# Optimization experiments

Hardware: AMD Instinct MI355X
Metric: run time of the kernel (lower is better)

The kernel has to match this reference:

```python
import jax, jax.numpy as jnp
import numpy as np

D = 512

def _linear(x, W, b):
    # torch Linear: x @ W.T + b, W is [out, in]
    return jnp.einsum('bnd,od->bno', x, W) + b

def _attend(Q, K, V):
    # scores: [B, N, N]
    s = jnp.einsum('bnd,bmd->bnm', Q, K)
    a = jax.nn.softmax(s, axis=-1)
    # F.normalize(p=1, dim=-1): divide by sum of abs (softmax is nonneg, sums to 1,
    # but stay faithful to the original math)
    a = a / jnp.clip(jnp.sum(jnp.abs(a), axis=-1, keepdims=True), 1e-12)
    a = a / jnp.sqrt(jnp.asarray(D, a.dtype))
    return jnp.einsum('bnm,bmd->bnd', a, V)

def setup_inputs() -> dict:
    key = jax.random.key(0)
    ks = jax.random.split(key, 12)
    B, N = 2, 4096
    lim = 1.0 / np.sqrt(D)
    lim2 = 1.0 / np.sqrt(2 * D)
    return {
        'x_f': jax.random.normal(ks[0], (B, N, D), jnp.float32),
        'x_s': jax.random.normal(ks[1], (B, N, D), jnp.float32),
        'Wq': jax.random.uniform(ks[2], (D, D), jnp.float32, -lim, lim),
        'bq': jax.random.uniform(ks[3], (D,), jnp.float32, -lim, lim),
        'Wk': jax.random.uniform(ks[4], (D, D), jnp.float32, -lim, lim),
        'bk': jax.random.uniform(ks[5], (D,), jnp.float32, -lim, lim),
        'Wv': jax.random.uniform(ks[6], (D, D), jnp.float32, -lim, lim),
        'bv': jax.random.uniform(ks[7], (D,), jnp.float32, -lim, lim),
        'Wc': jax.random.uniform(ks[8], (D, 2 * D), jnp.float32, -lim2, lim2),
        'bc': jax.random.uniform(ks[9], (D,), jnp.float32, -lim2, lim2),
    }

def reference(x_f, x_s, Wq, bq, Wk, bk, Wv, bv, Wc, bc):
    # dropout layers are identity in eval mode
    co_occur = jax.nn.relu(_linear(jnp.concatenate([x_f, x_s], axis=-1), Wc, bc))
    # f -> s direction
    out_f = _attend(_linear(x_f, Wq, bq), _linear(x_s, Wk, bk), _linear(x_f, Wv, bv)) + co_occur
    # s -> f direction
    out_s = _attend(_linear(x_s, Wq, bq), _linear(x_f, Wk, bk), _linear(x_s, Wv, bv)) + co_occur
    return (out_f, out_s)
```

## Files before the change

kernel.cpp:

```cpp
#include <hip/hip_runtime.h>
#include <stdint.h>


using bf16x8 = __attribute__((ext_vector_type(8))) short;
using f32x4  = __attribute__((ext_vector_type(4))) float;

typedef __attribute__((address_space(1))) const void as1_void_t;
typedef __attribute__((address_space(3))) void as3_void_t;

__device__ __forceinline__ void gload16(const void* g, void* l) {
  __builtin_amdgcn_global_load_lds((as1_void_t*)g, (as3_void_t*)l, 16, 0, 0);
}

#define BAR_VM0()                                                  \
  do {                                                             \
    asm volatile("s_waitcnt vmcnt(0) lgkmcnt(0)" ::: "memory");    \
    __builtin_amdgcn_s_barrier();                                  \
    __builtin_amdgcn_sched_barrier(0);                             \
  } while (0)

#define BAR_LGKM()                                                 \
  do {                                                             \
    asm volatile("s_waitcnt lgkmcnt(0)" ::: "memory");             \
    __builtin_amdgcn_s_barrier();                                  \
    __builtin_amdgcn_sched_barrier(0);                             \
  } while (0)

__device__ __forceinline__ unsigned f2bf_u(float f) {
  unsigned u = __float_as_uint(f);
  return (u + 0x7fffu + ((u >> 16) & 1u)) >> 16;
}

#define MFMA_BF16(a, b, c) __builtin_amdgcn_mfma_f32_16x16x32_bf16((a), (b), (c), 0, 0, 0)

__global__ void cvt_bf16(const float* __restrict__ src,
                         unsigned short* __restrict__ dst, int n4) {
  int i = blockIdx.x * blockDim.x + threadIdx.x;
  if (i >= n4) return;
  float4 v = ((const float4*)src)[i];
  uint2 o;
  o.x = f2bf_u(v.x) | (f2bf_u(v.y) << 16);
  o.y = f2bf_u(v.z) | (f2bf_u(v.w) << 16);
  ((uint2*)dst)[i] = o;
}

__global__ void split_wc(const float* __restrict__ Wc,
                         unsigned short* __restrict__ Wf,
                         unsigned short* __restrict__ Ws) {
  int t = blockIdx.x * blockDim.x + threadIdx.x;
  int row = t >> 7, col = (t & 127) * 4;
  float4 a = *(const float4*)(Wc + row * 1024 + col);
  float4 b = *(const float4*)(Wc + row * 1024 + 512 + col);
  uint2 oa, ob;
  oa.x = f2bf_u(a.x) | (f2bf_u(a.y) << 16);
  oa.y = f2bf_u(a.z) | (f2bf_u(a.w) << 16);
  ob.x = f2bf_u(b.x) | (f2bf_u(b.y) << 16);
  ob.y = f2bf_u(b.z) | (f2bf_u(b.w) << 16);
  *(uint2*)(Wf + row * 512 + col) = oa;
  *(uint2*)(Ws + row * 512 + col) = ob;
}

template<int EPI>
__global__ void __launch_bounds__(256)
gemm_proj(const unsigned short* __restrict__ A1,
          const unsigned short* __restrict__ A2,
          const unsigned short* __restrict__ W1,
          const unsigned short* __restrict__ W2,
          const float* __restrict__ bias,
          void* __restrict__ Cout, int nk) {
  __shared__ __align__(16) unsigned short As[2][128 * 32];
  __shared__ __align__(16) unsigned short Bs[2][128 * 32];
  const int tid = threadIdx.x;
  const int w = tid >> 6, lane = tid & 63;
  const int m0 = blockIdx.x * 128, n0 = blockIdx.y * 128;
  const int wm = (w >> 1) * 64, wn = (w & 1) * 64;
  f32x4 acc[4][4] = {};

  auto stage = [&](int ks, int bi) {
    const unsigned short* Ab = (EPI == 2 && ks >= 16) ? A2 : A1;
    const unsigned short* Wb = (EPI == 2 && ks >= 16) ? W2 : W1;
    const int k0 = (EPI == 2) ? ((ks & 15) * 32) : (ks * 32);
#pragma unroll
    for (int t = 0; t < 2; ++t) {
      const int o = t * 256 + tid;
      const int row = o >> 2, seg = o & 3;
      gload16(Ab + (size_t)(m0 + row) * 512 + k0 + seg * 8,
              (char*)As[bi] + t * 4096 + w * 1024);
      gload16(Wb + (size_t)(n0 + row) * 512 + k0 + seg * 8,
              (char*)Bs[bi] + t * 4096 + w * 1024);
    }
  };

  stage(0, 0);
  for (int ks = 0; ks < nk; ++ks) {
    const int bi = ks & 1;
    BAR_VM0();
    if (ks + 1 < nk) stage(ks + 1, bi ^ 1);
    bf16x8 a[4], b[4];
#pragma unroll
    for (int i = 0; i < 4; ++i) {
      a[i] = *(const bf16x8*)(As[bi] + (wm + i * 16 + (lane & 15)) * 32 + (lane >> 4) * 8);
      b[i] = *(const bf16x8*)(Bs[bi] + (wn + i * 16 + (lane & 15)) * 32 + (lane >> 4) * 8);
    }
#pragma unroll
    for (int i = 0; i < 4; ++i)
#pragma unroll
      for (int j = 0; j < 4; ++j)
        acc[i][j] = MFMA_BF16(a[i], b[j], acc[i][j]);
  }

  const int lm = lane >> 4, ln = lane & 15;
  if (EPI == 0) {
    unsigned short* Cb = (unsigned short*)Cout;
#pragma unroll
    for (int i = 0; i < 4; ++i)
#pragma unroll
      for (int j = 0; j < 4; ++j) {
        const int col = n0 + wn + j * 16 + ln;
        const float bv = bias[col];
#pragma unroll
        for (int r = 0; r < 4; ++r) {
          const int row = m0 + wm + i * 16 + lm * 4 + r;
          Cb[(size_t)row * 512 + col] = (unsigned short)f2bf_u(acc[i][j][r] + bv);
        }
      }
  } else if (EPI == 1) {
    unsigned short* Cb = (unsigned short*)Cout;
#pragma unroll
    for (int i = 0; i < 4; ++i)
#pragma unroll
      for (int j = 0; j < 4; ++j) {
        const int col = n0 + wn + j * 16 + ln;
        const float bv = bias[col];
#pragma unroll
        for (int r = 0; r < 4; ++r) {
          const int row = m0 + wm + i * 16 + lm * 4 + r;
          const int sb = row >> 12, n = row & 4095;
          Cb[(size_t)(sb * 512 + col) * 4096 + n] = (unsigned short)f2bf_u(acc[i][j][r] + bv);
        }
      }
  } else {
    float* Cb = (float*)Cout;
#pragma unroll
    for (int i = 0; i < 4; ++i)
#pragma unroll
      for (int j = 0; j < 4; ++j) {
        const int col = n0 + wn + j * 16 + ln;
        const float bv = bias[col];
#pragma unroll
        for (int r = 0; r < 4; ++r) {
          const int row = m0 + wm + i * 16 + lm * 4 + r;
          float v = acc[i][j][r] + bv;
          Cb[(size_t)row * 512 + col] = v > 0.f ? v : 0.f;
        }
      }
  }
}

__global__ void __launch_bounds__(512)
flash_attn(const unsigned short* __restrict__ Qb,
           const unsigned short* __restrict__ Kb,
           const unsigned short* __restrict__ Vt,
           const float* __restrict__ CO,
           float* __restrict__ Out) {
  __shared__ __align__(16) unsigned short Ks[2][32 * 512];
  __shared__ __align__(16) unsigned short Vs[2][512 * 32];
  __shared__ __align__(16) float S_lds[64 * 36];
  __shared__ __align__(16) unsigned short P_lds[64 * 48];
  __shared__ __align__(16) float m_run[64];
  __shared__ __align__(16) float l_run[64];
  __shared__ __align__(16) float alpha_l[64];

  const int tid = threadIdx.x;
  const int w = tid >> 6, lane = tid & 63;
  const int q0 = blockIdx.x * 64;
  const int b = blockIdx.y, dir = blockIdx.z;
  const int qw = w >> 1, kw = w & 1;

  const size_t qbase  = (size_t)(dir * 2 + b) * 4096 * 512;
  const size_t kbase  = (size_t)((1 - dir) * 2 + b) * 4096 * 512;
  const size_t vbase  = (size_t)(dir * 2 + b) * 512 * 4096;
  const size_t cobase = (size_t)b * 4096 * 512;
  const size_t obase  = qbase;

  auto stage_tiles = [&](int kt, int bi) {
    const int kv0 = kt * 32;
#pragma unroll
    for (int t = 0; t < 4; ++t) {
      const int krow = t * 8 + w;
      gload16(Kb + kbase + (size_t)(kv0 + krow) * 512 + (lane ^ (krow & 7)) * 8,
              (char*)Ks[bi] + krow * 1024);
      const int dbase = (t * 8 + w) * 16;
      const int d = dbase + (lane >> 2);
      gload16(Vt + vbase + (size_t)d * 4096 + kv0 + (((lane & 3) ^ (d & 3)) * 8),
              (char*)Vs[bi] + dbase * 64);
    }
  };

  if (tid < 64) { m_run[tid] = -1e30f; l_run[tid] = 0.0f; }

  stage_tiles(0, 0);

  bf16x8 qf[16];
  {
    const int qrow = q0 + qw * 16 + (lane & 15);
#pragma unroll
    for (int g = 0; g < 16; ++g)
      qf[g] = *(const bf16x8*)(Qb + qbase + (size_t)qrow * 512 + g * 32 + (lane >> 4) * 8);
  }

  f32x4 o_acc[4][4] = {};

  for (int kt = 0; kt < 128; ++kt) {
    const int bi = kt & 1;
    const unsigned short* Kc = Ks[bi];
    const unsigned short* Vc = Vs[bi];

    BAR_VM0();
    if (kt < 127) stage_tiles(kt + 1, bi ^ 1);

    {
      const int krow = kw * 16 + (lane & 15);
      f32x4 s0 = {}, s1 = {};
#pragma unroll
      for (int g = 0; g < 8; ++g) {
        const int c0 = (g * 4 + (lane >> 4)) ^ (krow & 7);
        const int c1 = ((g + 8) * 4 + (lane >> 4)) ^ (krow & 7);
        bf16x8 k0 = *(const bf16x8*)((const char*)Kc + krow * 1024 + c0 * 16);
        bf16x8 k1 = *(const bf16x8*)((const char*)Kc + krow * 1024 + c1 * 16);
        s0 = MFMA_BF16(qf[g], k0, s0);
        s1 = MFMA_BF16(qf[g + 8], k1, s1);
      }
      const int col = kw * 16 + (lane & 15);
      const int rb = qw * 16 + (lane >> 4) * 4;
#pragma unroll
      for (int r = 0; r < 4; ++r)
        S_lds[(rb + r) * 36 + col] = s0[r] + s1[r];
    }
    BAR_LGKM();

    {
      const int row = w * 8 + (lane >> 3);
      const int j = lane & 7;
      f32x4 sv = *(const f32x4*)&S_lds[row * 36 + j * 4];
      float mx = fmaxf(fmaxf(sv[0], sv[1]), fmaxf(sv[2], sv[3]));
      mx = fmaxf(mx, __shfl_xor(mx, 1));
      mx = fmaxf(mx, __shfl_xor(mx, 2));
      mx = fmaxf(mx, __shfl_xor(mx, 4));
      const float mold = m_run[row];
      const float mnew = fmaxf(mold, mx);
      float p0 = __expf(sv[0] - mnew), p1 = __expf(sv[1] - mnew);
      float p2 = __expf(sv[2] - mnew), p3 = __expf(sv[3] - mnew);
      float ls = p0 + p1 + p2 + p3;
      ls += __shfl_xor(ls, 1);
      ls += __shfl_xor(ls, 2);
      ls += __shfl_xor(ls, 4);
      const float alpha = __expf(mold - mnew);
      if (j == 0) {
        m_run[row] = mnew;
        l_run[row] = l_run[row] * alpha + ls;
        alpha_l[row] = alpha;
      }
      uint2 pw;
      pw.x = f2bf_u(p0) | (f2bf_u(p1) << 16);
      pw.y = f2bf_u(p2) | (f2bf_u(p3) << 16);
      *(uint2*)(P_lds + row * 48 + j * 4) = pw;
    }
    BAR_LGKM();

#pragma unroll
    for (int qi = 0; qi < 4; ++qi) {
      bf16x8 pa = *(const bf16x8*)(P_lds + (qi * 16 + (lane & 15)) * 48 + (lane >> 4) * 8);
      f32x4 al4 = *(const f32x4*)&alpha_l[qi * 16 + (lane >> 4) * 4];
#pragma unroll
      for (int di = 0; di < 4; ++di)
        o_acc[qi][di] *= al4;
#pragma unroll
      for (int di = 0; di < 4; ++di) {
        const int d = w * 64 + di * 16 + (lane & 15);
        const int slot = (lane >> 4) ^ (d & 3);
        bf16x8 vf = *(const bf16x8*)((const char*)Vc + d * 64 + slot * 16);
        o_acc[qi][di] = MFMA_BF16(pa, vf, o_acc[qi][di]);
      }
    }
  }

  BAR_LGKM();

  const float rsd = 0.04419417382415922f;
#pragma unroll
  for (int qi = 0; qi < 4; ++qi) {
#pragma unroll
    for (int r = 0; r < 4; ++r) {
      const int ql = qi * 16 + (lane >> 4) * 4 + r;
      const float inv = rsd / l_run[ql];
      const size_t rowoff = (size_t)(q0 + ql) * 512;
#pragma unroll
      for (int di = 0; di < 4; ++di) {
        const int d = w * 64 + di * 16 + (lane & 15);
        Out[obase + rowoff + d] = o_acc[qi][di][r] * inv + CO[cobase + rowoff + d];
      }
    }
  }
}

extern "C" void kernel_launch(void* const* d_in, const int* in_sizes, int n_in,
                              void* d_out, int out_size, void* d_ws, size_t ws_size,
                              hipStream_t stream) {
  const float* x_f = (const float*)d_in[0];
  const float* x_s = (const float*)d_in[1];
  const float* Wq  = (const float*)d_in[2];
  const float* bq  = (const float*)d_in[3];
  const float* Wk  = (const float*)d_in[4];
  const float* bk  = (const float*)d_in[5];
  const float* Wv  = (const float*)d_in[6];
  const float* bv  = (const float*)d_in[7];
  const float* Wc  = (const float*)d_in[8];
  const float* bc  = (const float*)d_in[9];
  float* out = (float*)d_out;

  unsigned short* Xb  = (unsigned short*)d_ws;
  unsigned short* Qb  = Xb + 8388608;
  unsigned short* Kb  = Qb + 8388608;
  unsigned short* Vt  = Kb + 8388608;
  float*          CO  = (float*)(Vt + 8388608);
  unsigned short* Wqb = (unsigned short*)(CO + 4194304);
  unsigned short* Wkb = Wqb + 262144;
  unsigned short* Wvb = Wkb + 262144;
  unsigned short* Wcf = Wvb + 262144;
  unsigned short* Wcs = Wcf + 262144;

  cvt_bf16<<<4096, 256, 0, stream>>>(x_f, Xb, 1048576);
  cvt_bf16<<<4096, 256, 0, stream>>>(x_s, Xb + 4194304, 1048576);
  cvt_bf16<<<256, 256, 0, stream>>>(Wq, Wqb, 65536);
  cvt_bf16<<<256, 256, 0, stream>>>(Wk, Wkb, 65536);
  cvt_bf16<<<256, 256, 0, stream>>>(Wv, Wvb, 65536);
  split_wc<<<256, 256, 0, stream>>>(Wc, Wcf, Wcs);

  dim3 gQ(128, 4);
  gemm_proj<0><<<gQ, 256, 0, stream>>>(Xb, nullptr, Wqb, nullptr, bq, Qb, 16);
  gemm_proj<0><<<gQ, 256, 0, stream>>>(Xb, nullptr, Wkb, nullptr, bk, Kb, 16);
  gemm_proj<1><<<gQ, 256, 0, stream>>>(Xb, nullptr, Wvb, nullptr, bv, Vt, 16);
  dim3 gC(64, 4);
  gemm_proj<2><<<gC, 256, 0, stream>>>(Xb, Xb + 4194304, Wcf, Wcs, bc, CO, 32);

  dim3 gF(64, 2, 2);
  flash_attn<<<gF, 512, 0, stream>>>(Qb, Kb, Vt, CO, out);
}
```

Measured before the change: 490.2 us.

## Halve flash-attention query tile, split QK over head-dim halves, load V directly

Shrinks the attention block from 64 to 32 query rows, which doubles the grid to 256 blocks and requests 4 blocks per CU via launch bounds. The QK^T product is split across two waves per tile along the head dimension, with partial scores summed in LDS. V fragments are now read straight from global memory into registers instead of being staged in double-buffered LDS, and K is single-buffered. Together these cut LDS and register use to raise occupancy. The cost is that each K/V tile is reread by twice as many blocks, V loads are exposed with no prefetch, and the K prefetch is serialised behind a barrier.

Result: slower. 640.6 us (+30.7%).

```diff
diff --git a/kernel.cpp b/kernel.cpp
--- a/kernel.cpp
+++ b/kernel.cpp
@@ -157,25 +157,24 @@
   }
 }
 
-__global__ void __launch_bounds__(512)
+__global__ void __launch_bounds__(512, 4)
 flash_attn(const unsigned short* __restrict__ Qb,
            const unsigned short* __restrict__ Kb,
            const unsigned short* __restrict__ Vt,
            const float* __restrict__ CO,
            float* __restrict__ Out) {
-  __shared__ __align__(16) unsigned short Ks[2][32 * 512];
-  __shared__ __align__(16) unsigned short Vs[2][512 * 32];
-  __shared__ __align__(16) float S_lds[64 * 36];
-  __shared__ __align__(16) unsigned short P_lds[64 * 48];
-  __shared__ __align__(16) float m_run[64];
-  __shared__ __align__(16) float l_run[64];
-  __shared__ __align__(16) float alpha_l[64];
+  __shared__ __align__(16) unsigned short Ks[32 * 512];
+  __shared__ __align__(16) float Sp[2][32][34];
+  __shared__ __align__(16) unsigned short P_lds[32 * 40];
+  __shared__ __align__(16) float m_run[32];
+  __shared__ __align__(16) float l_run[32];
+  __shared__ __align__(16) float alpha_l[32];
 
   const int tid = threadIdx.x;
   const int w = tid >> 6, lane = tid & 63;
-  const int q0 = blockIdx.x * 64;
+  const int q0 = blockIdx.x * 32;
   const int b = blockIdx.y, dir = blockIdx.z;
-  const int qw = w >> 1, kw = w & 1;
+  const int qw = (w >> 2) & 1, kw = (w >> 1) & 1, dh = w & 1;
 
   const size_t qbase  = (size_t)(dir * 2 + b) * 4096 * 512;
   const size_t kbase  = (size_t)((1 - dir) * 2 + b) * 4096 * 512;
@@ -183,113 +182,109 @@
   const size_t cobase = (size_t)b * 4096 * 512;
   const size_t obase  = qbase;
 
-  auto stage_tiles = [&](int kt, int bi) {
+  auto stage_k = [&](int kt) {
     const int kv0 = kt * 32;
 #pragma unroll
     for (int t = 0; t < 4; ++t) {
       const int krow = t * 8 + w;
       gload16(Kb + kbase + (size_t)(kv0 + krow) * 512 + (lane ^ (krow & 7)) * 8,
-              (char*)Ks[bi] + krow * 1024);
-      const int dbase = (t * 8 + w) * 16;
-      const int d = dbase + (lane >> 2);
-      gload16(Vt + vbase + (size_t)d * 4096 + kv0 + (((lane & 3) ^ (d & 3)) * 8),
-              (char*)Vs[bi] + dbase * 64);
+              (char*)Ks + krow * 1024);
     }
   };
 
-  if (tid < 64) { m_run[tid] = -1e30f; l_run[tid] = 0.0f; }
-
-  stage_tiles(0, 0);
-
-  bf16x8 qf[16];
+  if (tid < 32) { m_run[tid] = -1e30f; l_run[tid] = 0.0f; }
+
+  stage_k(0);
+
+  bf16x8 qf[8];
   {
     const int qrow = q0 + qw * 16 + (lane & 15);
 #pragma unroll
-    for (int g = 0; g < 16; ++g)
-      qf[g] = *(const bf16x8*)(Qb + qbase + (size_t)qrow * 512 + g * 32 + (lane >> 4) * 8);
-  }
-
-  f32x4 o_acc[4][4] = {};
+    for (int g = 0; g < 8; ++g)
+      qf[g] = *(const bf16x8*)(Qb + qbase + (size_t)qrow * 512 +
+                               dh * 256 + g * 32 + (lane >> 4) * 8);
+  }
+
+  f32x4 o_acc[2][4] = {};
 
   for (int kt = 0; kt < 128; ++kt) {
-    const int bi = kt & 1;
-    const unsigned short* Kc = Ks[bi];
-    const unsigned short* Vc = Vs[bi];
+    const int kv0 = kt * 32;
 
     BAR_VM0();
-    if (kt < 127) stage_tiles(kt + 1, bi ^ 1);
+
+    bf16x8 vf[4];
+#pragma unroll
+    for (int di = 0; di < 4; ++di) {
+      const int d = w * 64 + di * 16 + (lane & 15);
+      vf[di] = *(const bf16x8*)(Vt + vbase + (size_t)d * 4096 + kv0 + (lane >> 4) * 8);
+    }
 
     {
       const int krow = kw * 16 + (lane & 15);
       f32x4 s0 = {}, s1 = {};
 #pragma unroll
-      for (int g = 0; g < 8; ++g) {
-        const int c0 = (g * 4 + (lane >> 4)) ^ (krow & 7);
-        const int c1 = ((g + 8) * 4 + (lane >> 4)) ^ (krow & 7);
-        bf16x8 k0 = *(const bf16x8*)((const char*)Kc + krow * 1024 + c0 * 16);
-        bf16x8 k1 = *(const bf16x8*)((const char*)Kc + krow * 1024 + c1 * 16);
+      for (int g = 0; g < 4; ++g) {
+        const int c0 = (dh * 32 + g * 4 + (lane >> 4)) ^ (krow & 7);
+        const int c1 = (dh * 32 + (g + 4) * 4 + (lane >> 4)) ^ (krow & 7);
+        bf16x8 k0 = *(const bf16x8*)((const char*)Ks + krow * 1024 + c0 * 16);
+        bf16x8 k1 = *(const bf16x8*)((const char*)Ks + krow * 1024 + c1 * 16);
         s0 = MFMA_BF16(qf[g], k0, s0);
-        s1 = MFMA_BF16(qf[g + 8], k1, s1);
+        s1 = MFMA_BF16(qf[g + 4], k1, s1);
       }
       const int col = kw * 16 + (lane & 15);
       const int rb = qw * 16 + (lane >> 4) * 4;
 #pragma unroll
       for (int r = 0; r < 4; ++r)
-        S_lds[(rb + r) * 36 + col] = s0[r] + s1[r];
+        Sp[dh][rb + r][col] = s0[r] + s1[r];
     }
     BAR_LGKM();
+    if (kt < 127) stage_k(kt + 1);
 
     {
-      const int row = w * 8 + (lane >> 3);
-      const int j = lane & 7;
-      f32x4 sv = *(const f32x4*)&S_lds[row * 36 + j * 4];
-      float mx = fmaxf(fmaxf(sv[0], sv[1]), fmaxf(sv[2], sv[3]));
+      const int row = w * 4 + (lane >> 4);
+      const int j = lane & 15;
+      float2 a0 = *(const float2*)&Sp[0][row][j * 2];
+      float2 a1 = *(const float2*)&Sp[1][row][j * 2];
+      const float v0 = a0.x + a1.x, v1 = a0.y + a1.y;
+      float mx = fmaxf(v0, v1);
       mx = fmaxf(mx, __shfl_xor(mx, 1));
       mx = fmaxf(mx, __shfl_xor(mx, 2));
       mx = fmaxf(mx, __shfl_xor(mx, 4));
+      mx = fmaxf(mx, __shfl_xor(mx, 8));
       const float mold = m_run[row];
       const float mnew = fmaxf(mold, mx);
-      float p0 = __expf(sv[0] - mnew), p1 = __expf(sv[1] - mnew);
-      float p2 = __expf(sv[2] - mnew), p3 = __expf(sv[3] - mnew);
-      float ls = p0 + p1 + p2 + p3;
+      const float p0 = __expf(v0 - mnew), p1 = __expf(v1 - mnew);
+      float ls = p0 + p1;
       ls += __shfl_xor(ls, 1);
       ls += __shfl_xor(ls, 2);
       ls += __shfl_xor(ls, 4);
+      ls += __shfl_xor(ls, 8);
       const float alpha = __expf(mold - mnew);
       if (j == 0) {
         m_run[row] = mnew;
         l_run[row] = l_run[row] * alpha + ls;
         alpha_l[row] = alpha;
       }
-      uint2 pw;
-      pw.x = f2bf_u(p0) | (f2bf_u(p1) << 16);
-      pw.y = f2bf_u(p2) | (f2bf_u(p3) << 16);
-      *(uint2*)(P_lds + row * 48 + j * 4) = pw;
+      *(unsigned*)(P_lds + row * 40 + j * 2) = f2bf_u(p0) | (f2bf_u(p1) << 16);
     }
     BAR_LGKM();
 
 #pragma unroll
-    for (int qi = 0; qi < 4; ++qi) {
-      bf16x8 pa = *(const bf16x8*)(P_lds + (qi * 16 + (lane & 15)) * 48 + (lane >> 4) * 8);
+    for (int qi = 0; qi < 2; ++qi) {
+      bf16x8 pf = *(const bf16x8*)(P_lds + (qi * 16 + (lane & 15)) * 40 + (lane >> 4) * 8);
       f32x4 al4 = *(const f32x4*)&alpha_l[qi * 16 + (lane >> 4) * 4];
 #pragma unroll
       for (int di = 0; di < 4; ++di)
         o_acc[qi][di] *= al4;
 #pragma unroll
-      for (int di = 0; di < 4; ++di) {
-        const int d = w * 64 + di * 16 + (lane & 15);
-        const int slot = (lane >> 4) ^ (d & 3);
-        bf16x8 vf = *(const bf16x8*)((const char*)Vc + d * 64 + slot * 16);
-        o_acc[qi][di] = MFMA_BF16(pa, vf, o_acc[qi][di]);
-      }
-    }
-  }
-
-  BAR_LGKM();
+      for (int di = 0; di < 4; ++di)
+        o_acc[qi][di] = MFMA_BF16(pf, vf[di], o_acc[qi][di]);
+    }
+  }
 
   const float rsd = 0.04419417382415922f;
 #pragma unroll
-  for (int qi = 0; qi < 4; ++qi) {
+  for (int qi = 0; qi < 2; ++qi) {
 #pragma unroll
     for (int r = 0; r < 4; ++r) {
       const int ql = qi * 16 + (lane >> 4) * 4 + r;
@@ -344,6 +339,6 @@
   dim3 gC(64, 4);
   gemm_proj<2><<<gC, 256, 0, stream>>>(Xb, Xb + 4194304, Wcf, Wcs, bc, CO, 32);
 
-  dim3 gF(64, 2, 2);
+  dim3 gF(128, 2, 2);
   flash_attn<<<gF, 512, 0, stream>>>(Qb, Kb, Vt, CO, out);
 }
```

## Fuse QKV projections and restructure attention to keep scores in registers

Applied to the files above, without the earlier changes.

Merges the three Q/K/V projection GEMMs into one launch over a concatenated weight buffer (Wq, Wk and Wv are contiguous in the workspace), choosing bias and output layout per column segment. In the attention kernel, each wave now computes full-depth scores for its own 16x16 query/key block and does the softmax in registers. Only per-row max and sum partials are exchanged through LDS, which removes the S_lds round-trip. V tiles are no longer staged through LDS; each wave reads its V fragments straight from global memory. This removes LDS traffic and one pass of reduction work, but V reads become unpipelined global loads that may expose latency.

Result: faster. 474.3 us (-3.2%).

```diff
diff --git a/kernel.cpp b/kernel.cpp
--- a/kernel.cpp
+++ b/kernel.cpp
@@ -60,14 +60,83 @@
   *(uint2*)(Ws + row * 512 + col) = ob;
 }
 
-template<int EPI>
 __global__ void __launch_bounds__(256)
-gemm_proj(const unsigned short* __restrict__ A1,
-          const unsigned short* __restrict__ A2,
-          const unsigned short* __restrict__ W1,
-          const unsigned short* __restrict__ W2,
-          const float* __restrict__ bias,
-          void* __restrict__ Cout, int nk) {
+gemm_qkv(const unsigned short* __restrict__ Xb,
+         const unsigned short* __restrict__ Wall,
+         const float* __restrict__ bq, const float* __restrict__ bk,
+         const float* __restrict__ bv,
+         unsigned short* __restrict__ Qb, unsigned short* __restrict__ Kb,
+         unsigned short* __restrict__ Vt) {
+  __shared__ __align__(16) unsigned short As[2][128 * 32];
+  __shared__ __align__(16) unsigned short Bs[2][128 * 32];
+  const int tid = threadIdx.x;
+  const int w = tid >> 6, lane = tid & 63;
+  const int m0 = blockIdx.x * 128, n0 = blockIdx.y * 128;
+  const int seg = n0 >> 9, c0 = n0 & 511;
+  const int wm = (w >> 1) * 64, wn = (w & 1) * 64;
+  f32x4 acc[4][4] = {};
+
+  auto stage = [&](int ks, int bi) {
+    const int k0 = ks * 32;
+#pragma unroll
+    for (int t = 0; t < 2; ++t) {
+      const int o = t * 256 + tid;
+      const int row = o >> 2, sg = o & 3;
+      gload16(Xb + (size_t)(m0 + row) * 512 + k0 + sg * 8,
+              (char*)As[bi] + t * 4096 + w * 1024);
+      gload16(Wall + (size_t)(n0 + row) * 512 + k0 + sg * 8,
+              (char*)Bs[bi] + t * 4096 + w * 1024);
+    }
+  };
+
+  stage(0, 0);
+  for (int ks = 0; ks < 16; ++ks) {
+    const int bi = ks & 1;
+    BAR_VM0();
+    if (ks + 1 < 16) stage(ks + 1, bi ^ 1);
+    bf16x8 a[4], b[4];
+#pragma unroll
+    for (int i = 0; i < 4; ++i) {
+      a[i] = *(const bf16x8*)(As[bi] + (wm + i * 16 + (lane & 15)) * 32 + (lane >> 4) * 8);
+      b[i] = *(const bf16x8*)(Bs[bi] + (wn + i * 16 + (lane & 15)) * 32 + (lane >> 4) * 8);
+    }
+#pragma unroll
+    for (int i = 0; i < 4; ++i)
+#pragma unroll
+      for (int j = 0; j < 4; ++j)
+        acc[i][j] = MFMA_BF16(a[i], b[j], acc[i][j]);
+  }
+
+  const int lm = lane >> 4, ln = lane & 15;
+  const float* bias = (seg == 0) ? bq : (seg == 1) ? bk : bv;
+  unsigned short* flatout = (seg == 0) ? Qb : Kb;
+#pragma unroll
+  for (int i = 0; i < 4; ++i)
+#pragma unroll
+    for (int j = 0; j < 4; ++j) {
+      const int c = c0 + wn + j * 16 + ln;
+      const float bvv = bias[c];
+#pragma unroll
+      for (int r = 0; r < 4; ++r) {
+        const int row = m0 + wm + i * 16 + lm * 4 + r;
+        const unsigned short val = (unsigned short)f2bf_u(acc[i][j][r] + bvv);
+        if (seg < 2) {
+          flatout[(size_t)row * 512 + c] = val;
+        } else {
+          const int sb = row >> 12, n = row & 4095;
+          Vt[(size_t)(sb * 512 + c) * 4096 + n] = val;
+        }
+      }
+    }
+}
+
+__global__ void __launch_bounds__(256)
+gemm_co(const unsigned short* __restrict__ A1,
+        const unsigned short* __restrict__ A2,
+        const unsigned short* __restrict__ W1,
+        const unsigned short* __restrict__ W2,
+        const float* __restrict__ bias,
+        float* __restrict__ Cout) {
   __shared__ __align__(16) unsigned short As[2][128 * 32];
   __shared__ __align__(16) unsigned short Bs[2][128 * 32];
   const int tid = threadIdx.x;
@@ -77,25 +146,25 @@
   f32x4 acc[4][4] = {};
 
   auto stage = [&](int ks, int bi) {
-    const unsigned short* Ab = (EPI == 2 && ks >= 16) ? A2 : A1;
-    const unsigned short* Wb = (EPI == 2 && ks >= 16) ? W2 : W1;
-    const int k0 = (EPI == 2) ? ((ks & 15) * 32) : (ks * 32);
+    const unsigned short* Ab = (ks >= 16) ? A2 : A1;
+    const unsigned short* Wb = (ks >= 16) ? W2 : W1;
+    const int k0 = (ks & 15) * 32;
 #pragma unroll
     for (int t = 0; t < 2; ++t) {
       const int o = t * 256 + tid;
-      const int row = o >> 2, seg = o & 3;
-      gload16(Ab + (size_t)(m0 + row) * 512 + k0 + seg * 8,
+      const int row = o >> 2, sg = o & 3;
+      gload16(Ab + (size_t)(m0 + row) * 512 + k0 + sg * 8,
               (char*)As[bi] + t * 4096 + w * 1024);
-      gload16(Wb + (size_t)(n0 + row) * 512 + k0 + seg * 8,
+      gload16(Wb + (size_t)(n0 + row) * 512 + k0 + sg * 8,
               (char*)Bs[bi] + t * 4096 + w * 1024);
     }
   };
 
   stage(0, 0);
-  for (int ks = 0; ks < nk; ++ks) {
+  for (int ks = 0; ks < 32; ++ks) {
     const int bi = ks & 1;
     BAR_VM0();
-    if (ks + 1 < nk) stage(ks + 1, bi ^ 1);
+    if (ks + 1 < 32) stage(ks + 1, bi ^ 1);
     bf16x8 a[4], b[4];
 #pragma unroll
     for (int i = 0; i < 4; ++i) {
@@ -110,51 +179,19 @@
   }
 
   const int lm = lane >> 4, ln = lane & 15;
-  if (EPI == 0) {
-    unsigned short* Cb = (unsigned short*)Cout;
-#pragma unroll
-    for (int i = 0; i < 4; ++i)
-#pragma unroll
-      for (int j = 0; j < 4; ++j) {
-        const int col = n0 + wn + j * 16 + ln;
-        const float bv = bias[col];
-#pragma unroll
-        for (int r = 0; r < 4; ++r) {
-          const int row = m0 + wm + i * 16 + lm * 4 + r;
-          Cb[(size_t)row * 512 + col] = (unsigned short)f2bf_u(acc[i][j][r] + bv);
-        }
+#pragma unroll
+  for (int i = 0; i < 4; ++i)
+#pragma unroll
+    for (int j = 0; j < 4; ++j) {
+      const int col = n0 + wn + j * 16 + ln;
+      const float bvv = bias[col];
+#pragma unroll
+      for (int r = 0; r < 4; ++r) {
+        const int row = m0 + wm + i * 16 + lm * 4 + r;
+        float v = acc[i][j][r] + bvv;
+        Cout[(size_t)row * 512 + col] = v > 0.f ? v : 0.f;
       }
-  } else if (EPI == 1) {
-    unsigned short* Cb = (unsigned short*)Cout;
-#pragma unroll
-    for (int i = 0; i < 4; ++i)
-#pragma unroll
-      for (int j = 0; j < 4; ++j) {
-        const int col = n0 + wn + j * 16 + ln;
-        const float bv = bias[col];
-#pragma unroll
-        for (int r = 0; r < 4; ++r) {
-          const int row = m0 + wm + i * 16 + lm * 4 + r;
-          const int sb = row >> 12, n = row & 4095;
-          Cb[(size_t)(sb * 512 + col) * 4096 + n] = (unsigned short)f2bf_u(acc[i][j][r] + bv);
-        }
-      }
-  } else {
-    float* Cb = (float*)Cout;
-#pragma unroll
-    for (int i = 0; i < 4; ++i)
-#pragma unroll
-      for (int j = 0; j < 4; ++j) {
-        const int col = n0 + wn + j * 16 + ln;
-        const float bv = bias[col];
-#pragma unroll
-        for (int r = 0; r < 4; ++r) {
-          const int row = m0 + wm + i * 16 + lm * 4 + r;
-          float v = acc[i][j][r] + bv;
-          Cb[(size_t)row * 512 + col] = v > 0.f ? v : 0.f;
-        }
-      }
-  }
+    }
 }
 
 __global__ void __launch_bounds__(512)
@@ -164,9 +201,9 @@
            const float* __restrict__ CO,
            float* __restrict__ Out) {
   __shared__ __align__(16) unsigned short Ks[2][32 * 512];
-  __shared__ __align__(16) unsigned short Vs[2][512 * 32];
-  __shared__ __align__(16) float S_lds[64 * 36];
   __shared__ __align__(16) unsigned short P_lds[64 * 48];
+  __shared__ __align__(16) float pmax[2][64];
+  __shared__ __align__(16) float psum[2][64];
   __shared__ __align__(16) float m_run[64];
   __shared__ __align__(16) float l_run[64];
   __shared__ __align__(16) float alpha_l[64];
@@ -175,7 +212,8 @@
   const int w = tid >> 6, lane = tid & 63;
   const int q0 = blockIdx.x * 64;
   const int b = blockIdx.y, dir = blockIdx.z;
-  const int qw = w >> 1, kw = w & 1;
+  const int qs = w & 3, kt = w >> 2;
+  const int qcol = qs * 16 + (lane & 15);
 
   const size_t qbase  = (size_t)(dir * 2 + b) * 4096 * 512;
   const size_t kbase  = (size_t)((1 - dir) * 2 + b) * 4096 * 512;
@@ -183,27 +221,23 @@
   const size_t cobase = (size_t)b * 4096 * 512;
   const size_t obase  = qbase;
 
-  auto stage_tiles = [&](int kt, int bi) {
-    const int kv0 = kt * 32;
+  auto stage_k = [&](int t_, int bi) {
+    const int kv0 = t_ * 32;
 #pragma unroll
     for (int t = 0; t < 4; ++t) {
       const int krow = t * 8 + w;
       gload16(Kb + kbase + (size_t)(kv0 + krow) * 512 + (lane ^ (krow & 7)) * 8,
               (char*)Ks[bi] + krow * 1024);
-      const int dbase = (t * 8 + w) * 16;
-      const int d = dbase + (lane >> 2);
-      gload16(Vt + vbase + (size_t)d * 4096 + kv0 + (((lane & 3) ^ (d & 3)) * 8),
-              (char*)Vs[bi] + dbase * 64);
     }
   };
 
   if (tid < 64) { m_run[tid] = -1e30f; l_run[tid] = 0.0f; }
 
-  stage_tiles(0, 0);
+  stage_k(0, 0);
 
   bf16x8 qf[16];
   {
-    const int qrow = q0 + qw * 16 + (lane & 15);
+    const int qrow = q0 + qcol;
 #pragma unroll
     for (int g = 0; g < 16; ++g)
       qf[g] = *(const bf16x8*)(Qb + qbase + (size_t)qrow * 512 + g * 32 + (lane >> 4) * 8);
@@ -211,77 +245,76 @@
 
   f32x4 o_acc[4][4] = {};
 
-  for (int kt = 0; kt < 128; ++kt) {
-    const int bi = kt & 1;
-    const unsigned short* Kc = Ks[bi];
-    const unsigned short* Vc = Vs[bi];
+  for (int it = 0; it < 128; ++it) {
+    const int cur = it & 1;
+    const int kv0 = it * 32;
 
     BAR_VM0();
-    if (kt < 127) stage_tiles(kt + 1, bi ^ 1);
-
+
+    bf16x8 vf[4];
+#pragma unroll
+    for (int di = 0; di < 4; ++di) {
+      const int d = w * 64 + di * 16 + (lane & 15);
+      vf[di] = *(const bf16x8*)(Vt + vbase + (size_t)d * 4096 + kv0 + (lane >> 4) * 8);
+    }
+    if (it < 127) stage_k(it + 1, cur ^ 1);
+
+    const float m_old = m_run[qcol];
+
+    f32x4 sa[4] = {{}, {}, {}, {}};
     {
-      const int krow = kw * 16 + (lane & 15);
-      f32x4 s0 = {}, s1 = {};
-#pragma unroll
-      for (int g = 0; g < 8; ++g) {
-        const int c0 = (g * 4 + (lane >> 4)) ^ (krow & 7);
-        const int c1 = ((g + 8) * 4 + (lane >> 4)) ^ (krow & 7);
-        bf16x8 k0 = *(const bf16x8*)((const char*)Kc + krow * 1024 + c0 * 16);
-        bf16x8 k1 = *(const bf16x8*)((const char*)Kc + krow * 1024 + c1 * 16);
-        s0 = MFMA_BF16(qf[g], k0, s0);
-        s1 = MFMA_BF16(qf[g + 8], k1, s1);
+      const int krow = kt * 16 + (lane & 15);
+#pragma unroll
+      for (int g = 0; g < 16; ++g) {
+        const int c = (g * 4 + (lane >> 4)) ^ (krow & 7);
+        bf16x8 kf = *(const bf16x8*)((const char*)Ks[cur] + krow * 1024 + c * 16);
+        sa[g & 3] = MFMA_BF16(kf, qf[g], sa[g & 3]);
       }
-      const int col = kw * 16 + (lane & 15);
-      const int rb = qw * 16 + (lane >> 4) * 4;
-#pragma unroll
-      for (int r = 0; r < 4; ++r)
-        S_lds[(rb + r) * 36 + col] = s0[r] + s1[r];
-    }
+    }
+    f32x4 s;
+#pragma unroll
+    for (int r = 0; r < 4; ++r) s[r] = (sa[0][r] + sa[1][r]) + (sa[2][r] + sa[3][r]);
+
+    float mx = fmaxf(fmaxf(s[0], s[1]), fmaxf(s[2], s[3]));
+    mx = fmaxf(mx, __shfl_xor(mx, 16));
+    mx = fmaxf(mx, __shfl_xor(mx, 32));
+    if (lane < 16) pmax[kt][qs * 16 + lane] = mx;
     BAR_LGKM();
-
+    const float m_tile = fmaxf(mx, pmax[kt ^ 1][qcol]);
+    const float m_new = fmaxf(m_old, m_tile);
+    const float alpha = __expf(m_old - m_new);
+    float p0 = __expf(s[0] - m_new), p1 = __expf(s[1] - m_new);
+    float p2 = __expf(s[2] - m_new), p3 = __expf(s[3] - m_new);
+    float ls = (p0 + p1) + (p2 + p3);
+    ls += __shfl_xor(ls, 16);
+    ls += __shfl_xor(ls, 32);
+    if (lane < 16) psum[kt][qs * 16 + lane] = ls;
+    if (kt == 0 && lane < 16) {
+      m_run[qs * 16 + lane] = m_new;
+      alpha_l[qs * 16 + lane] = alpha;
+    }
     {
-      const int row = w * 8 + (lane >> 3);
-      const int j = lane & 7;
-      f32x4 sv = *(const f32x4*)&S_lds[row * 36 + j * 4];
-      float mx = fmaxf(fmaxf(sv[0], sv[1]), fmaxf(sv[2], sv[3]));
-      mx = fmaxf(mx, __shfl_xor(mx, 1));
-      mx = fmaxf(mx, __shfl_xor(mx, 2));
-      mx = fmaxf(mx, __shfl_xor(mx, 4));
-      const float mold = m_run[row];
-      const float mnew = fmaxf(mold, mx);
-      float p0 = __expf(sv[0] - mnew), p1 = __expf(sv[1] - mnew);
-      float p2 = __expf(sv[2] - mnew), p3 = __expf(sv[3] - mnew);
-      float ls = p0 + p1 + p2 + p3;
-      ls += __shfl_xor(ls, 1);
-      ls += __shfl_xor(ls, 2);
-      ls += __shfl_xor(ls, 4);
-      const float alpha = __expf(mold - mnew);
-      if (j == 0) {
-        m_run[row] = mnew;
-        l_run[row] = l_run[row] * alpha + ls;
-        alpha_l[row] = alpha;
-      }
       uint2 pw;
       pw.x = f2bf_u(p0) | (f2bf_u(p1) << 16);
       pw.y = f2bf_u(p2) | (f2bf_u(p3) << 16);
-      *(uint2*)(P_lds + row * 48 + j * 4) = pw;
+      *(uint2*)(P_lds + qcol * 48 + kt * 16 + (lane >> 4) * 4) = pw;
     }
     BAR_LGKM();
 
 #pragma unroll
     for (int qi = 0; qi < 4; ++qi) {
-      bf16x8 pa = *(const bf16x8*)(P_lds + (qi * 16 + (lane & 15)) * 48 + (lane >> 4) * 8);
+      bf16x8 pf = *(const bf16x8*)(P_lds + (qi * 16 + (lane & 15)) * 48 + (lane >> 4) * 8);
       f32x4 al4 = *(const f32x4*)&alpha_l[qi * 16 + (lane >> 4) * 4];
 #pragma unroll
       for (int di = 0; di < 4; ++di)
         o_acc[qi][di] *= al4;
 #pragma unroll
-      for (int di = 0; di < 4; ++di) {
-        const int d = w * 64 + di * 16 + (lane & 15);
-        const int slot = (lane >> 4) ^ (d & 3);
-        bf16x8 vf = *(const bf16x8*)((const char*)Vc + d * 64 + slot * 16);
-        o_acc[qi][di] = MFMA_BF16(pa, vf, o_acc[qi][di]);
-      }
+      for (int di = 0; di < 4; ++di)
+        o_acc[qi][di] = MFMA_BF16(pf, vf[di], o_acc[qi][di]);
+    }
+    if (kt == 1 && lane < 16) {
+      const int q_ = qs * 16 + lane;
+      l_run[q_] = l_run[q_] * alpha + psum[0][q_] + psum[1][q_];
     }
   }
 
@@ -337,12 +370,10 @@
   cvt_bf16<<<256, 256, 0, stream>>>(Wv, Wvb, 65536);
   split_wc<<<256, 256, 0, stream>>>(Wc, Wcf, Wcs);
 
-  dim3 gQ(128, 4);
-  gemm_proj<0><<<gQ, 256, 0, stream>>>(Xb, nullptr, Wqb, nullptr, bq, Qb, 16);
-  gemm_proj<0><<<gQ, 256, 0, stream>>>(Xb, nullptr, Wkb, nullptr, bk, Kb, 16);
-  gemm_proj<1><<<gQ, 256, 0, stream>>>(Xb, nullptr, Wvb, nullptr, bv, Vt, 16);
+  dim3 gQKV(128, 12);
+  gemm_qkv<<<gQKV, 256, 0, stream>>>(Xb, Wqb, bq, bk, bv, Qb, Kb, Vt);
   dim3 gC(64, 4);
-  gemm_proj<2><<<gC, 256, 0, stream>>>(Xb, Xb + 4194304, Wcf, Wcs, bc, CO, 32);
+  gemm_co<<<gC, 256, 0, stream>>>(Xb, Xb + 4194304, Wcf, Wcs, bc, CO);
 
   dim3 gF(64, 2, 2);
   flash_attn<<<gF, 512, 0, stream>>>(Qb, Kb, Vt, CO, out);
```
